# Kernel tuning notes

Hardware: AMD Instinct MI355X
Metric: run time of the kernel (lower is better)

Reference implementation:

```python
import jax, jax.numpy as jnp
import numpy as np

L, P = 8, 512
HID = 128
N_COARSE, N_FINE = 64, 128
LVIS_NEAR, LVIS_FAR = 1e-3, 0.5
S = 100.0  # 1 / fixed_s_recp


def _mlp_sdf(x, w0, b0, w1, b1, w2, b2, w3, b3):
    # x: [..., 3] -> sdf [...]
    h = jax.nn.relu(x @ w0 + b0)
    h = jax.nn.relu(h @ w1 + b1)
    h = jax.nn.relu(h @ w2 + b2)
    return (h @ w3 + b3)[..., 0]


def _sdf_to_w(sdf, s):
    # faithful to sdf_to_w: cdf -> alpha -> visibility weights via cumprod
    cdf = jax.nn.sigmoid(sdf * s)
    alpha = jnp.clip((cdf[..., :-1] - cdf[..., 1:]) / (cdf[..., :-1] + 1e-10), 0.0, None)
    ones = jnp.ones(alpha.shape[:-1] + (1,), alpha.dtype)
    shifted = jnp.concatenate([ones, 1.0 - alpha + 1e-10], axis=-1)
    return alpha * jnp.cumprod(shifted, axis=-1)[..., :-1]


def _sample_pdf(bins, weights, u):
    # standard NeRF importance sampling; bins [...,M+1], weights [...,M], u [...,N]
    weights = weights + 1e-5
    pdf = weights / jnp.sum(weights, axis=-1, keepdims=True)
    cdf = jnp.cumsum(pdf, axis=-1)
    cdf = jnp.concatenate([jnp.zeros_like(cdf[..., :1]), cdf], axis=-1)  # [...,M+1]
    # searchsorted (right) via broadcast compare: [...,N,M+1]
    inds = jnp.sum((u[..., None] >= cdf[..., None, :]).astype(jnp.int32), axis=-1)
    below = jnp.clip(inds - 1, 0, cdf.shape[-1] - 1)
    above = jnp.clip(inds, 0, cdf.shape[-1] - 1)
    cdf_b = jnp.take_along_axis(cdf, below, axis=-1)
    cdf_a = jnp.take_along_axis(cdf, above, axis=-1)
    bins_b = jnp.take_along_axis(bins, below, axis=-1)
    bins_a = jnp.take_along_axis(bins, above, axis=-1)
    denom = cdf_a - cdf_b
    denom = jnp.where(denom < 1e-5, jnp.ones_like(denom), denom)
    t = (u - cdf_b) / denom
    return bins_b + t * (bins_a - bins_b)


def setup_inputs() -> dict:
    key = jax.random.key(0)
    ks = jax.random.split(key, 8)

    def lin(k, fi, fo):
        return jax.random.normal(k, (fi, fo), jnp.float32) / jnp.sqrt(jnp.float32(fi))

    return {
        "pts": jax.random.normal(ks[0], (1, P, 3), jnp.float32) * 0.5,
        "light_posi": jax.random.normal(ks[1], (L, 3), jnp.float32) * 2.0,
        "u": jax.random.uniform(ks[2], (L, P, N_FINE), jnp.float32),
        "w0": lin(ks[3], 3, HID), "b0": jnp.zeros((HID,), jnp.float32),
        "w1": lin(ks[4], HID, HID), "b1": jnp.zeros((HID,), jnp.float32),
        "w2": lin(ks[5], HID, HID), "b2": jnp.zeros((HID,), jnp.float32),
        "w3": lin(ks[6], HID, 1), "b3": jnp.zeros((1,), jnp.float32),
    }


def reference(pts, light_posi, u, w0, b0, w1, b1, w2, b2, w3, b3):
    sdf = lambda x: _mlp_sdf(x, w0, b0, w1, b1, w2, b2, w3, b3)
    # pts: [1,P,3]; light_posi: [L,3]
    pts2l = light_posi[:, None, :] - pts  # [L,P,3]
    pts2l = pts2l / jnp.linalg.norm(pts2l, axis=-1, keepdims=True)
    t = jnp.linspace(0.0, 1.0 - 1.0 / N_COARSE, N_COARSE, dtype=jnp.float32)
    d_coarse = LVIS_NEAR * (1.0 - t) + LVIS_FAR * t  # [N_COARSE]
    d_coarse = jnp.broadcast_to(d_coarse, (pts2l.shape[0], pts.shape[1], N_COARSE))
    # coarse sample points: [L,P,Nc,3]
    pts_coarse = pts[:, :, None, :] + d_coarse[..., None] * pts2l[:, :, None, :]
    w_coarse = _sdf_to_w(sdf(pts_coarse), S)  # [L,P,Nc-1]
    d_fine = _sample_pdf(d_coarse, w_coarse, u)  # [L,P,Nf]
    d_all = jnp.sort(jnp.concatenate([d_coarse, d_fine], axis=-1), axis=-1)  # [L,P,Nc+Nf]
    pts_all = pts[:, :, None, :] + d_all[..., None] * pts2l[:, :, None, :]
    w_all = _sdf_to_w(sdf(pts_all), S)
    occu = jnp.sum(w_all, axis=-1)  # [L,P]
    return 1.0 - occu
```

## Files before the change

### kernel.cpp

```cpp
#include <hip/hip_runtime.h>
#include <math.h>

#define NL 8
#define NP 512
#define NC 64
#define NF 128
#define NALL 192
#define NRAY (NL * NP)
#define HID 128

typedef _Float16 half8 __attribute__((ext_vector_type(8)));
typedef _Float16 half4v __attribute__((ext_vector_type(4)));
typedef float floatx16 __attribute__((ext_vector_type(16)));
typedef unsigned long long ull;

#define MFMA(a, b, c) __builtin_amdgcn_mfma_f32_32x32x16_f16((a), (b), (c), 0, 0, 0)


__device__ __forceinline__ float dcoarse_at(int i) {
    float t = (float)i * 0.015625f;
    return 1e-3f * (1.0f - t) + 0.5f * t;
}

__device__ __forceinline__ floatx16 fzero16() {
    floatx16 z;
#pragma unroll
    for (int i = 0; i < 16; ++i) z[i] = 0.f;
    return z;
}
__device__ __forceinline__ half8 hzero8() {
    half8 z;
#pragma unroll
    for (int i = 0; i < 8; ++i) z[i] = (_Float16)0.f;
    return z;
}

__global__ void prep_kernel(const float* __restrict__ w1, const float* __restrict__ w2,
                            _Float16* __restrict__ Wsp) {
    int f = blockIdx.x * 256 + threadIdx.x;
    int layer = blockIdx.y;
    const float* w = layer ? w2 : w1;
    int i = f & 7, l31 = (f >> 3) & 31, lhi = (f >> 8) & 1, ks = (f >> 9) & 7, jb = f >> 12;
    int j = jb * 32 + l31;
    int k = ks * 16 + lhi * 8 + i;
    float v = w[k * 128 + j];
    _Float16 hi = (_Float16)v;
    Wsp[(layer * 2 + 0) * 16384 + f] = hi;
    Wsp[(layer * 2 + 1) * 16384 + f] = (_Float16)(v - (float)hi);
}

template<int MODE, int FASTW>
__global__ __launch_bounds__(512, 4) void mlp_kernel(
    const float* __restrict__ pts, const float* __restrict__ lights,
    const float* __restrict__ d_fine,
    const float* __restrict__ w0, const float* __restrict__ b0,
    const float* __restrict__ w1, const float* __restrict__ b1,
    const float* __restrict__ w2, const float* __restrict__ b2,
    const float* __restrict__ w3, const float* __restrict__ b3,
    const _Float16* __restrict__ Wsp,
    float* __restrict__ sdf_out)
{
    __shared__ __align__(16) _Float16 Hhi[128 * 128];
    __shared__ __align__(16) _Float16 Hlo[128 * 128];
    __shared__ _Float16 Xs[6 * 128];
    __shared__ float P2[4 * 128];

    const int tid = threadIdx.x;
    const int lane = tid & 63;
    const int wv = tid >> 6;
    const int jq = wv & 3, mh = wv >> 2;
    const int l31 = lane & 31, lhi = lane >> 5;
    const int base = blockIdx.x * 128;

    if (tid < 128) {
        int pt = base + tid;
        int ray; float d;
        if (MODE == 0) { ray = pt >> 6; d = dcoarse_at(pt & 63); }
        else           { ray = pt >> 7; d = d_fine[pt]; }
        int l = ray >> 9, p = ray & (NP - 1);
        float px = pts[p * 3 + 0], py = pts[p * 3 + 1], pz = pts[p * 3 + 2];
        float dx = lights[l * 3 + 0] - px, dy = lights[l * 3 + 1] - py, dz = lights[l * 3 + 2] - pz;
        float n = sqrtf(dx * dx + dy * dy + dz * dz);
        dx /= n; dy /= n; dz /= n;
        float xc[3] = { px + d * dx, py + d * dy, pz + d * dz };
#pragma unroll
        for (int c = 0; c < 3; ++c) {
            _Float16 h = (_Float16)xc[c];
            Xs[c * 128 + tid] = h;
            Xs[(3 + c) * 128 + tid] = (_Float16)(xc[c] - (float)h);
        }
    }
    __syncthreads();

    const int m0 = mh * 64;

    auto haddr = [&](int m, int k0) {
        return m * 128 + ((((k0 >> 3) ^ (m & 15)) << 3) | (k0 & 7));
    };

    auto store_tile = [&](const floatx16& a, int mt, const float* __restrict__ bias) {
        int m = m0 + mt * 32 + l31;
#pragma unroll
        for (int g = 0; g < 4; ++g) {
            int jg = jq * 32 + 8 * g + 4 * lhi;
            half4v hq, lq;
#pragma unroll
            for (int q = 0; q < 4; ++q) {
                float v = fmaxf(a[g * 4 + q] + bias[jg + q], 0.f);
                _Float16 hi = (_Float16)v;
                hq[q] = hi;
                lq[q] = (_Float16)(v - (float)hi);
            }
            int ad = haddr(m, jg);
            *(half4v*)&Hhi[ad] = hq;
            *(half4v*)&Hlo[ad] = lq;
        }
    };

    floatx16 acc[2];

    auto ldA = [&](int L, int ks, half8& ah, half8& al) {
        if (FASTW) {
            int off = (((jq * 8 + ks) * 2 + lhi) * 32 + l31) * 8;
            ah = *(const half8*)&Wsp[(L * 2 + 0) * 16384 + off];
            al = *(const half8*)&Wsp[(L * 2 + 1) * 16384 + off];
        } else {
            const float* w = L ? w2 : w1;
            int j = jq * 32 + l31, k0 = ks * 16 + lhi * 8;
#pragma unroll
            for (int i = 0; i < 8; ++i) {
                float v = w[(k0 + i) * 128 + j];
                _Float16 hi = (_Float16)v;
                ah[i] = hi;
                al[i] = (_Float16)(v - (float)hi);
            }
        }
    };

    {
        half8 a1h = hzero8(), a1l = hzero8(), bh1[2], bl1[2];
        bh1[0] = hzero8(); bh1[1] = hzero8(); bl1[0] = hzero8(); bl1[1] = hzero8();
        if (lhi == 0) {
            int j = jq * 32 + l31;
#pragma unroll
            for (int c = 0; c < 3; ++c) {
                float v = w0[c * 128 + j];
                _Float16 hi = (_Float16)v;
                a1h[c] = hi;
                a1l[c] = (_Float16)(v - (float)hi);
            }
#pragma unroll
            for (int mt = 0; mt < 2; ++mt) {
                int m = m0 + mt * 32 + l31;
#pragma unroll
                for (int c = 0; c < 3; ++c) {
                    bh1[mt][c] = Xs[c * 128 + m];
                    bl1[mt][c] = Xs[(3 + c) * 128 + m];
                }
            }
        }
        acc[0] = fzero16(); acc[1] = fzero16();
        acc[0] = MFMA(a1l, bh1[0], acc[0]); acc[1] = MFMA(a1l, bh1[1], acc[1]);
        acc[0] = MFMA(a1h, bl1[0], acc[0]); acc[1] = MFMA(a1h, bl1[1], acc[1]);
        acc[0] = MFMA(a1h, bh1[0], acc[0]); acc[1] = MFMA(a1h, bh1[1], acc[1]);
        store_tile(acc[0], 0, b0);
        store_tile(acc[1], 1, b0);
    }

    auto gemm = [&](int L, half8 pa_h, half8 pa_l) {
        acc[0] = fzero16(); acc[1] = fzero16();
#pragma unroll
        for (int ks = 0; ks < 8; ++ks) {
            half8 ah, al;
            if (ks == 0) { ah = pa_h; al = pa_l; }
            else         ldA(L, ks, ah, al);
            half8 bh[2], bl[2];
#pragma unroll
            for (int mt = 0; mt < 2; ++mt) {
                int ad = haddr(m0 + mt * 32 + l31, ks * 16 + lhi * 8);
                bh[mt] = *(const half8*)&Hhi[ad];
                bl[mt] = *(const half8*)&Hlo[ad];
            }
            acc[0] = MFMA(al, bh[0], acc[0]); acc[1] = MFMA(al, bh[1], acc[1]);
            acc[0] = MFMA(ah, bl[0], acc[0]); acc[1] = MFMA(ah, bl[1], acc[1]);
            acc[0] = MFMA(ah, bh[0], acc[0]); acc[1] = MFMA(ah, bh[1], acc[1]);
        }
    };

    half8 pfh, pfl;
    ldA(0, 0, pfh, pfl);
    __syncthreads();

    gemm(0, pfh, pfl);
    ldA(1, 0, pfh, pfl);
    __syncthreads();
    store_tile(acc[0], 0, b1);
    store_tile(acc[1], 1, b1);
    __syncthreads();

    gemm(1, pfh, pfl);
#pragma unroll
    for (int mt = 0; mt < 2; ++mt) {
        float p = 0.f;
#pragma unroll
        for (int g = 0; g < 4; ++g) {
            int jg = jq * 32 + 8 * g + 4 * lhi;
#pragma unroll
            for (int q = 0; q < 4; ++q) {
                float v = fmaxf(acc[mt][g * 4 + q] + b2[jg + q], 0.f);
                p = fmaf(v, w3[jg + q], p);
            }
        }
        p += __shfl_xor(p, 32);
        if (lane < 32) P2[jq * 128 + m0 + mt * 32 + l31] = p;
    }
    __syncthreads();
    if (tid < 128)
        sdf_out[base + tid] = b3[0] + P2[tid] + P2[128 + tid] + P2[256 + tid] + P2[384 + tid];
}

__global__ __launch_bounds__(256) void sample_kernel(
    const float* __restrict__ sdf_c, const float* __restrict__ u,
    float* __restrict__ d_fine, unsigned char* __restrict__ perm8) {
    const int lane = threadIdx.x & 63, wv = threadIdx.x >> 6;
    const int ray = blockIdx.x * 4 + wv;

    float sv = sdf_c[ray * NC + lane];
    float c = 1.0f / (1.0f + expf(-100.0f * sv));
    float cn = __shfl_down(c, 1);
    bool valid = lane < 63;
    float a = valid ? fmaxf((c - cn) / (c + 1e-10f), 0.f) : 0.f;
    float sh = valid ? (1.f - a + 1e-10f) : 1.f;
    float ps = sh;
#pragma unroll
    for (int off = 1; off < 64; off <<= 1) { float o = __shfl_up(ps, off); if (lane >= off) ps *= o; }
    float T = __shfl_up(ps, 1);
    if (lane == 0) T = 1.f;
    float w = valid ? (a * T + 1e-5f) : 0.f;
    float wsum = w;
#pragma unroll
    for (int off = 1; off < 64; off <<= 1) wsum += __shfl_xor(wsum, off);
    float pdf = w / wsum;
    float cs = pdf;
#pragma unroll
    for (int off = 1; off < 64; off <<= 1) { float o = __shfl_up(cs, off); if (lane >= off) cs += o; }
    float cdfv = __shfl_up(cs, 1);
    if (lane == 0) cdfv = 0.f;

    float df[2];
#pragma unroll
    for (int t = 0; t < 2; ++t) {
        float uu = u[ray * NF + t * 64 + lane];
        int lo = 0;
#pragma unroll
        for (int b = 32; b >= 1; b >>= 1) {
            float cm = __shfl(cdfv, lo + b);
            if (uu >= cm) lo += b;
        }
        int above = min(lo + 1, NC - 1);
        float cb = __shfl(cdfv, lo), ca = __shfl(cdfv, above);
        float bb = dcoarse_at(lo), ba = dcoarse_at(above);
        float denom = ca - cb;
        if (denom < 1e-5f) denom = 1.f;
        float tt = (uu - cb) / denom;
        df[t] = bb + tt * (ba - bb);
        d_fine[ray * 128 + t * 64 + lane] = df[t];
    }

    ull v[4];
    v[0] = ((ull)__float_as_uint(dcoarse_at(lane)) << 32) | (unsigned)lane;
    v[1] = ((ull)__float_as_uint(df[0]) << 32) | (unsigned)(64 + lane);
    v[2] = ((ull)__float_as_uint(df[1]) << 32) | (unsigned)(128 + lane);
    v[3] = ((ull)0x7F800000u << 32) | 255u;
    for (int k = 2; k <= 256; k <<= 1) {
        for (int j = k >> 1; j > 0; j >>= 1) {
            if (j >= 64) {
                int tj = j >> 6;
#pragma unroll
                for (int t = 0; t < 4; ++t) {
                    if ((t & tj) == 0) {
                        int t2 = t ^ tj;
                        bool asc = (((t * 64) & k) == 0);
                        ull x = v[t], y = v[t2];
                        bool sw = asc ? (x > y) : (x < y);
                        if (sw) { v[t] = y; v[t2] = x; }
                    }
                }
            } else {
#pragma unroll
                for (int t = 0; t < 4; ++t) {
                    int i = t * 64 + lane;
                    ull other = __shfl_xor(v[t], j);
                    bool lower = (lane & j) == 0;
                    bool asc = ((i & k) == 0);
                    bool takeMin = (lower == asc);
                    ull mn = v[t] < other ? v[t] : other;
                    ull mx = v[t] < other ? other : v[t];
                    v[t] = takeMin ? mn : mx;
                }
            }
        }
    }
#pragma unroll
    for (int t = 0; t < 3; ++t)
        perm8[ray * NALL + t * 64 + lane] = (unsigned char)(v[t] & 0xFFu);
}

__global__ __launch_bounds__(256) void finish_kernel(
    const float* __restrict__ sdf_c, const float* __restrict__ sdf_f,
    const unsigned char* __restrict__ perm8, float* __restrict__ out) {
    int lane = threadIdx.x & 63, wv = threadIdx.x >> 6;
    int ray = blockIdx.x * 4 + wv;
    const unsigned char* P = perm8 + (size_t)ray * NALL;
    float c[4];
#pragma unroll
    for (int t = 0; t < 4; ++t) {
        int i = lane * 3 + t;
        if (i < NALL) {
            int idx = P[i];
            float s = (idx < 64) ? sdf_c[ray * NC + idx] : sdf_f[ray * 128 + (idx - 64)];
            c[t] = 1.0f / (1.0f + expf(-100.0f * s));
        } else c[t] = 0.f;
    }
    float a[3], s[3];
#pragma unroll
    for (int t = 0; t < 3; ++t) {
        int i = lane * 3 + t;
        if (i < NALL - 1) {
            a[t] = fmaxf((c[t] - c[t + 1]) / (c[t] + 1e-10f), 0.f);
            s[t] = 1.f - a[t] + 1e-10f;
        } else { a[t] = 0.f; s[t] = 1.f; }
    }
    float chunk = s[0] * s[1] * s[2];
    float ps = chunk;
#pragma unroll
    for (int off = 1; off < 64; off <<= 1) {
        float o = __shfl_up(ps, off);
        if (lane >= off) ps *= o;
    }
    float T = __shfl_up(ps, 1);
    if (lane == 0) T = 1.f;
    float occ = a[0] * T;
    T *= s[0]; occ = fmaf(a[1], T, occ);
    T *= s[1]; occ = fmaf(a[2], T, occ);
#pragma unroll
    for (int off = 1; off < 64; off <<= 1) occ += __shfl_xor(occ, off);
    if (lane == 0) out[ray] = 1.f - occ;
}

extern "C" void kernel_launch(void* const* d_in, const int* in_sizes, int n_in,
                              void* d_out, int out_size, void* d_ws, size_t ws_size,
                              hipStream_t stream) {
    const float* pts = (const float*)d_in[0];
    const float* lights = (const float*)d_in[1];
    const float* u = (const float*)d_in[2];
    const float* w0 = (const float*)d_in[3];
    const float* b0 = (const float*)d_in[4];
    const float* w1 = (const float*)d_in[5];
    const float* b1 = (const float*)d_in[6];
    const float* w2 = (const float*)d_in[7];
    const float* b2 = (const float*)d_in[8];
    const float* w3 = (const float*)d_in[9];
    const float* b3 = (const float*)d_in[10];
    float* out = (float*)d_out;

    char* wsb = (char*)d_ws;
    float* sdf_c = (float*)wsb;
    float* sdf_f = (float*)(wsb + (size_t)NRAY * NC * 4);
    float* d_fine = (float*)(wsb + (size_t)NRAY * (NC + 128) * 4);
    unsigned char* perm8 = (unsigned char*)(wsb + (size_t)NRAY * (NC + 256) * 4);
    _Float16* Wsp = (_Float16*)(wsb + (size_t)NRAY * (NC + 256) * 4 + (size_t)NRAY * NALL);
    const size_t need = (size_t)NRAY * (NC + 256) * 4 + (size_t)NRAY * NALL
                      + (size_t)4 * 16384 * sizeof(_Float16);
    const bool fast = ws_size >= need;

    if (fast) {
        prep_kernel<<<dim3(64, 2), 256, 0, stream>>>(w1, w2, Wsp);
        mlp_kernel<0, 1><<<(NRAY * NC) / 128, 512, 0, stream>>>(
            pts, lights, nullptr, w0, b0, w1, b1, w2, b2, w3, b3, Wsp, sdf_c);
        sample_kernel<<<NRAY / 4, 256, 0, stream>>>(sdf_c, u, d_fine, perm8);
        mlp_kernel<1, 1><<<(NRAY * 128) / 128, 512, 0, stream>>>(
            pts, lights, d_fine, w0, b0, w1, b1, w2, b2, w3, b3, Wsp, sdf_f);
    } else {
        mlp_kernel<0, 0><<<(NRAY * NC) / 128, 512, 0, stream>>>(
            pts, lights, nullptr, w0, b0, w1, b1, w2, b2, w3, b3, nullptr, sdf_c);
        sample_kernel<<<NRAY / 4, 256, 0, stream>>>(sdf_c, u, d_fine, perm8);
        mlp_kernel<1, 0><<<(NRAY * 128) / 128, 512, 0, stream>>>(
            pts, lights, d_fine, w0, b0, w1, b1, w2, b2, w3, b3, nullptr, sdf_f);
    }
    finish_kernel<<<NRAY / 4, 256, 0, stream>>>(sdf_c, sdf_f, perm8, out);
}
```

Baseline: 241.4 us.

## Remap MLP warp tiling to share B fragments across two output-column tiles

```diff
diff --git a/kernel.cpp b/kernel.cpp
--- a/kernel.cpp
+++ b/kernel.cpp
@@ -60,15 +60,14 @@
     const _Float16* __restrict__ Wsp,
     float* __restrict__ sdf_out)
 {
-    __shared__ __align__(16) _Float16 Hhi[128 * 128];
-    __shared__ __align__(16) _Float16 Hlo[128 * 128];
+    __shared__ __align__(16) _Float16 H[2 * 128 * 128];
     __shared__ _Float16 Xs[6 * 128];
-    __shared__ float P2[4 * 128];
+    __shared__ float P2[2 * 128];
 
     const int tid = threadIdx.x;
     const int lane = tid & 63;
     const int wv = tid >> 6;
-    const int jq = wv & 3, mh = wv >> 2;
+    const int jh = wv & 1, mq = wv >> 1;
     const int l31 = lane & 31, lhi = lane >> 5;
     const int base = blockIdx.x * 128;
 
@@ -90,19 +89,22 @@
             Xs[(3 + c) * 128 + tid] = (_Float16)(xc[c] - (float)h);
         }
     }
-    __syncthreads();
-
-    const int m0 = mh * 64;
-
-    auto haddr = [&](int m, int k0) {
-        return m * 128 + ((((k0 >> 3) ^ (m & 15)) << 3) | (k0 & 7));
-    };
-
-    auto store_tile = [&](const floatx16& a, int mt, const float* __restrict__ bias) {
-        int m = m0 + mt * 32 + l31;
+
+    const int m0 = mq * 32;
+    const int mrow = m0 + l31;
+    char* Hb = (char*)H;
+
+    int rdoff[8];
+#pragma unroll
+    for (int ks = 0; ks < 8; ++ks) {
+        int k0 = ks * 16 + lhi * 8;
+        rdoff[ks] = (mrow * 128 + ((((k0 >> 3) ^ (mrow & 15)) << 3) | (k0 & 7))) * 2;
+    }
+
+    auto store_tile = [&](const floatx16& a, int jt, const float* __restrict__ bias) {
 #pragma unroll
         for (int g = 0; g < 4; ++g) {
-            int jg = jq * 32 + 8 * g + 4 * lhi;
+            int jg = jh * 64 + jt * 32 + 8 * g + 4 * lhi;
             half4v hq, lq;
 #pragma unroll
             for (int q = 0; q < 4; ++q) {
@@ -111,112 +113,135 @@
                 hq[q] = hi;
                 lq[q] = (_Float16)(v - (float)hi);
             }
-            int ad = haddr(m, jg);
-            *(half4v*)&Hhi[ad] = hq;
-            *(half4v*)&Hlo[ad] = lq;
+            int ad = (mrow * 128 + ((((jg >> 3) ^ (mrow & 15)) << 3) | (jg & 7))) * 2;
+            *(half4v*)(Hb + ad) = hq;
+            *(half4v*)(Hb + ad + 32768) = lq;
         }
     };
 
     floatx16 acc[2];
 
-    auto ldA = [&](int L, int ks, half8& ah, half8& al) {
-        if (FASTW) {
-            int off = (((jq * 8 + ks) * 2 + lhi) * 32 + l31) * 8;
-            ah = *(const half8*)&Wsp[(L * 2 + 0) * 16384 + off];
-            al = *(const half8*)&Wsp[(L * 2 + 1) * 16384 + off];
-        } else {
-            const float* w = L ? w2 : w1;
-            int j = jq * 32 + l31, k0 = ks * 16 + lhi * 8;
-#pragma unroll
-            for (int i = 0; i < 8; ++i) {
-                float v = w[(k0 + i) * 128 + j];
-                _Float16 hi = (_Float16)v;
-                ah[i] = hi;
-                al[i] = (_Float16)(v - (float)hi);
-            }
+    const int aoff = lhi * 256 + l31 * 8 + 2048;
+    const _Float16* pA00h = Wsp + 0 * 16384 + (jh * 2 + 0) * 4096 + aoff;
+    const _Float16* pA00l = Wsp + 1 * 16384 + (jh * 2 + 0) * 4096 + aoff;
+    const _Float16* pA01h = Wsp + 0 * 16384 + (jh * 2 + 1) * 4096 + aoff;
+    const _Float16* pA01l = Wsp + 1 * 16384 + (jh * 2 + 1) * 4096 + aoff;
+    const _Float16* pA10h = Wsp + 2 * 16384 + (jh * 2 + 0) * 4096 + aoff;
+    const _Float16* pA10l = Wsp + 3 * 16384 + (jh * 2 + 0) * 4096 + aoff;
+    const _Float16* pA11h = Wsp + 2 * 16384 + (jh * 2 + 1) * 4096 + aoff;
+    const _Float16* pA11l = Wsp + 3 * 16384 + (jh * 2 + 1) * 4096 + aoff;
+
+    auto ldA_slow = [&](int L, int jt, int ks, half8& ah, half8& al) {
+        const float* w = L ? w2 : w1;
+        int j = jh * 64 + jt * 32 + l31, k0 = ks * 16 + lhi * 8;
+#pragma unroll
+        for (int i = 0; i < 8; ++i) {
+            float v = w[(k0 + i) * 128 + j];
+            _Float16 hi = (_Float16)v;
+            ah[i] = hi;
+            al[i] = (_Float16)(v - (float)hi);
         }
     };
 
+    auto gemm = [&](int L, const _Float16* p0h, const _Float16* p0l,
+                    const _Float16* p1h, const _Float16* p1l,
+                    half8 pf0h, half8 pf0l, half8 pf1h, half8 pf1l) {
+        acc[0] = fzero16(); acc[1] = fzero16();
+#pragma unroll
+        for (int ks = 0; ks < 8; ++ks) {
+            half8 bh = *(const half8*)(Hb + rdoff[ks]);
+            half8 bl = *(const half8*)(Hb + rdoff[ks] + 32768);
+            half8 a0h, a0l, a1h, a1l;
+            if (FASTW) {
+                if (ks == 0) { a0h = pf0h; a0l = pf0l; a1h = pf1h; a1l = pf1l; }
+                else {
+                    a0h = *(const half8*)(p0h + ks * 512 - 2048);
+                    a0l = *(const half8*)(p0l + ks * 512 - 2048);
+                    a1h = *(const half8*)(p1h + ks * 512 - 2048);
+                    a1l = *(const half8*)(p1l + ks * 512 - 2048);
+                }
+            } else {
+                ldA_slow(L, 0, ks, a0h, a0l);
+                ldA_slow(L, 1, ks, a1h, a1l);
+            }
+            acc[0] = MFMA(a0l, bh, acc[0]); acc[1] = MFMA(a1l, bh, acc[1]);
+            acc[0] = MFMA(a0h, bl, acc[0]); acc[1] = MFMA(a1h, bl, acc[1]);
+            acc[0] = MFMA(a0h, bh, acc[0]); acc[1] = MFMA(a1h, bh, acc[1]);
+        }
+    };
+
+    __syncthreads();
+
     {
-        half8 a1h = hzero8(), a1l = hzero8(), bh1[2], bl1[2];
-        bh1[0] = hzero8(); bh1[1] = hzero8(); bl1[0] = hzero8(); bl1[1] = hzero8();
+        half8 a1h[2], a1l[2], bh1 = hzero8(), bl1 = hzero8();
+        a1h[0] = hzero8(); a1h[1] = hzero8(); a1l[0] = hzero8(); a1l[1] = hzero8();
         if (lhi == 0) {
-            int j = jq * 32 + l31;
+#pragma unroll
+            for (int jt = 0; jt < 2; ++jt) {
+                int j = jh * 64 + jt * 32 + l31;
+#pragma unroll
+                for (int c = 0; c < 3; ++c) {
+                    float v = w0[c * 128 + j];
+                    _Float16 hi = (_Float16)v;
+                    a1h[jt][c] = hi;
+                    a1l[jt][c] = (_Float16)(v - (float)hi);
+                }
+            }
 #pragma unroll
             for (int c = 0; c < 3; ++c) {
-                float v = w0[c * 128 + j];
-                _Float16 hi = (_Float16)v;
-                a1h[c] = hi;
-                a1l[c] = (_Float16)(v - (float)hi);
-            }
-#pragma unroll
-            for (int mt = 0; mt < 2; ++mt) {
-                int m = m0 + mt * 32 + l31;
-#pragma unroll
-                for (int c = 0; c < 3; ++c) {
-                    bh1[mt][c] = Xs[c * 128 + m];
-                    bl1[mt][c] = Xs[(3 + c) * 128 + m];
-                }
+                bh1[c] = Xs[c * 128 + mrow];
+                bl1[c] = Xs[(3 + c) * 128 + mrow];
             }
         }
         acc[0] = fzero16(); acc[1] = fzero16();
-        acc[0] = MFMA(a1l, bh1[0], acc[0]); acc[1] = MFMA(a1l, bh1[1], acc[1]);
-        acc[0] = MFMA(a1h, bl1[0], acc[0]); acc[1] = MFMA(a1h, bl1[1], acc[1]);
-        acc[0] = MFMA(a1h, bh1[0], acc[0]); acc[1] = MFMA(a1h, bh1[1], acc[1]);
+        acc[0] = MFMA(a1l[0], bh1, acc[0]); acc[1] = MFMA(a1l[1], bh1, acc[1]);
+        acc[0] = MFMA(a1h[0], bl1, acc[0]); acc[1] = MFMA(a1h[1], bl1, acc[1]);
+        acc[0] = MFMA(a1h[0], bh1, acc[0]); acc[1] = MFMA(a1h[1], bh1, acc[1]);
         store_tile(acc[0], 0, b0);
         store_tile(acc[1], 1, b0);
     }
 
-    auto gemm = [&](int L, half8 pa_h, half8 pa_l) {
-        acc[0] = fzero16(); acc[1] = fzero16();
-#pragma unroll
-        for (int ks = 0; ks < 8; ++ks) {
-            half8 ah, al;
-            if (ks == 0) { ah = pa_h; al = pa_l; }
-            else         ldA(L, ks, ah, al);
-            half8 bh[2], bl[2];
-#pragma unroll
-            for (int mt = 0; mt < 2; ++mt) {
-                int ad = haddr(m0 + mt * 32 + l31, ks * 16 + lhi * 8);
-                bh[mt] = *(const half8*)&Hhi[ad];
-                bl[mt] = *(const half8*)&Hlo[ad];
-            }
-            acc[0] = MFMA(al, bh[0], acc[0]); acc[1] = MFMA(al, bh[1], acc[1]);
-            acc[0] = MFMA(ah, bl[0], acc[0]); acc[1] = MFMA(ah, bl[1], acc[1]);
-            acc[0] = MFMA(ah, bh[0], acc[0]); acc[1] = MFMA(ah, bh[1], acc[1]);
-        }
-    };
-
-    half8 pfh, pfl;
-    ldA(0, 0, pfh, pfl);
+    half8 pf0h, pf0l, pf1h, pf1l;
+    if (FASTW) {
+        pf0h = *(const half8*)(pA00h - 2048);
+        pf0l = *(const half8*)(pA00l - 2048);
+        pf1h = *(const half8*)(pA01h - 2048);
+        pf1l = *(const half8*)(pA01l - 2048);
+    }
     __syncthreads();
 
-    gemm(0, pfh, pfl);
-    ldA(1, 0, pfh, pfl);
+    gemm(0, pA00h, pA00l, pA01h, pA01l, pf0h, pf0l, pf1h, pf1l);
+    if (FASTW) {
+        pf0h = *(const half8*)(pA10h - 2048);
+        pf0l = *(const half8*)(pA10l - 2048);
+        pf1h = *(const half8*)(pA11h - 2048);
+        pf1l = *(const half8*)(pA11l - 2048);
+    }
     __syncthreads();
     store_tile(acc[0], 0, b1);
     store_tile(acc[1], 1, b1);
     __syncthreads();
 
-    gemm(1, pfh, pfl);
-#pragma unroll
-    for (int mt = 0; mt < 2; ++mt) {
+    gemm(1, pA10h, pA10l, pA11h, pA11l, pf0h, pf0l, pf1h, pf1l);
+    {
         float p = 0.f;
 #pragma unroll
-        for (int g = 0; g < 4; ++g) {
-            int jg = jq * 32 + 8 * g + 4 * lhi;
-#pragma unroll
-            for (int q = 0; q < 4; ++q) {
-                float v = fmaxf(acc[mt][g * 4 + q] + b2[jg + q], 0.f);
-                p = fmaf(v, w3[jg + q], p);
-            }
-        }
+        for (int jt = 0; jt < 2; ++jt)
+#pragma unroll
+            for (int g = 0; g < 4; ++g) {
+                int jg = jh * 64 + jt * 32 + 8 * g + 4 * lhi;
+#pragma unroll
+                for (int q = 0; q < 4; ++q) {
+                    float v = fmaxf(acc[jt][g * 4 + q] + b2[jg + q], 0.f);
+                    p = fmaf(v, w3[jg + q], p);
+                }
+            }
         p += __shfl_xor(p, 32);
-        if (lane < 32) P2[jq * 128 + m0 + mt * 32 + l31] = p;
+        if (lane < 32) P2[jh * 128 + mrow] = p;
     }
     __syncthreads();
     if (tid < 128)
-        sdf_out[base + tid] = b3[0] + P2[tid] + P2[128 + tid] + P2[256 + tid] + P2[384 + tid];
+        sdf_out[base + tid] = b3[0] + P2[tid] + P2[128 + tid];
 }
 
 __global__ __launch_bounds__(256) void sample_kernel(
```

Result: slower. 268.9 us (+11.4%).
